# Kernel optimization log

Hardware: AMD Instinct MI355X
Metric: run time of the kernel (lower is better)

Reference implementation:

```python
import jax, jax.numpy as jnp
import numpy as np

N = 100000      # number of edge features (rows of feats)
M = 800000      # number of triplets
HID = 128
HEADS = 8
DH = HID // HEADS


def setup_inputs() -> dict:
    key = jax.random.key(0)
    ks = jax.random.split(key, 10)
    s = 1.0 / np.sqrt(HID)
    inp = {
        "feats": jax.random.normal(ks[0], (N, HID), dtype=jnp.float32),
        "idx_kj": jax.random.randint(ks[1], (M,), 0, N, dtype=jnp.int64),
        "idx_ji": jax.random.randint(ks[2], (M,), 0, N, dtype=jnp.int64),
        "Wv": jax.random.uniform(ks[3], (HID, HID), jnp.float32, -s, s),
        "Wq": jax.random.uniform(ks[4], (HID, HID), jnp.float32, -s, s),
        "Wk": jax.random.uniform(ks[5], (HID, HID), jnp.float32, -s, s),
        "W1": jax.random.uniform(ks[6], (HID, HID), jnp.float32, -s, s),
        "b1": jax.random.uniform(ks[7], (HID,), jnp.float32, -s, s),
        "W2": jax.random.uniform(ks[8], (HID, HID), jnp.float32, -s, s),
        "b2": jax.random.uniform(ks[9], (HID,), jnp.float32, -s, s),
    }
    return inp


def reference(feats, idx_kj, idx_ji, Wv, Wq, Wk, W1, b1, W2, b2):
    # Projections (no bias), reshape to [N, H, Dh]
    v = (feats @ Wv.T).reshape(N, HEADS, DH)
    k = (feats @ Wk.T).reshape(N, HEADS, DH)
    q = (feats @ Wq.T).reshape(N, HEADS, DH)

    # edge-indexed attention scores: [M, H, 1]
    att = jnp.sum(q[idx_kj] * k[idx_ji], axis=-1, keepdims=True)
    att = jnp.exp(jax.nn.leaky_relu(att, negative_slope=0.2))  # unsafe softmax, as in source

    # segment-sum normalizer over destination index idx_ji: [N, H, 1]
    denom = jax.ops.segment_sum(att, idx_ji, num_segments=N)
    att = att / denom[idx_ji]

    # weighted V gather-scatter: [M, HID] -> [N, HID]
    v_att = (v[idx_kj] * att).reshape(M, HID)
    agg = jax.ops.segment_sum(v_att, idx_ji, num_segments=N)  # v_clone after +scatter-v

    v_flat = v.reshape(N, HID)
    # ResidualLayer (dropout in eval mode -> identity): v + relu(lin2(relu(lin1(agg))))
    h = jax.nn.relu(agg @ W1.T + b1)
    h = jax.nn.relu(h @ W2.T + b2)
    return v_flat + h
```

## Files before the change

kernel.cpp:

```cpp
#include <hip/hip_runtime.h>
#include <hip/hip_bf16.h>
#include <math.h>

#define N_NODES 100000
#define M_EDGES 800000
#define HID 128
#define HEADS 8
#define DH 16
#define SCAN_NB ((N_NODES + 1023) / 1024)
#define DBINS 64

typedef __attribute__((ext_vector_type(8))) short short8;
typedef __attribute__((ext_vector_type(4))) float floatx4;

__device__ __forceinline__ ushort f32_to_bf16(float x) {
    __hip_bfloat16 h = __float2bfloat16(x);
    union { __hip_bfloat16 h; ushort u; } c; c.h = h;
    return c.u;
}
__device__ __forceinline__ float bf16_bits_to_f32(ushort u) {
    union { unsigned int i; float f; } c; c.i = ((unsigned int)u) << 16;
    return c.f;
}
__device__ __forceinline__ float bf16pair_lo(unsigned int p) {
    union { unsigned int i; float f; } c; c.i = p << 16; return c.f;
}
__device__ __forceinline__ float bf16pair_hi(unsigned int p) {
    union { unsigned int i; float f; } c; c.i = p & 0xffff0000u; return c.f;
}

__device__ __forceinline__ void stage_w_frag(const ushort* __restrict__ W,
                                             ushort* __restrict__ lds, int tid)
{
    #pragma unroll
    for (int i = 0; i < 8; ++i) {
        int idx  = i * 256 + tid;
        int f    = idx >> 6;
        int lane = idx & 63;
        int t    = f & 7, ks = f >> 3;
        int row  = t * 16 + (lane & 15);
        int col  = ks * 32 + (lane >> 4) * 8;
        uint4 d = *(const uint4*)(W + row * HID + col);
        *(uint4*)(lds + idx * 8) = d;
    }
}

__global__ __launch_bounds__(256) void cvt_w_kernel(
    const float* __restrict__ Wq, const float* __restrict__ Wk, const float* __restrict__ Wv,
    const float* __restrict__ W1, const float* __restrict__ W2,
    ushort* __restrict__ dq, ushort* __restrict__ dk, ushort* __restrict__ dv,
    ushort* __restrict__ d1, ushort* __restrict__ d2)
{
    int i = blockIdx.x * 256 + threadIdx.x;
    int w = i >> 14;
    int j = i & 16383;
    const float* s[5] = {Wq, Wk, Wv, W1, W2};
    ushort*      d[5] = {dq, dk, dv, d1, d2};
    d[w][j] = f32_to_bf16(s[w][j]);
}

__global__ __launch_bounds__(256) void qkv_mfma_kernel(
    const float* __restrict__ feats,
    const ushort* __restrict__ Wq16, const ushort* __restrict__ Wk16, const ushort* __restrict__ Wv16,
    ushort* __restrict__ qv16, ushort* __restrict__ k16)
{
    __shared__ ushort wlds[16384];
    const int tid  = threadIdx.x;
    const int wave = tid >> 6;
    const int lane = tid & 63;
    const int row0 = blockIdx.x * 128 + wave * 32;
    const int lrow = lane & 15;
    const int lk   = (lane >> 4) * 8;
    const int crow = (lane >> 4) * 4;

    short8 afrag[2][4];
    bool tvalid[2];
    #pragma unroll
    for (int r = 0; r < 2; ++r) {
        int rr = row0 + r * 16;
        tvalid[r] = (rr < N_NODES);
        const float* arow = feats + (size_t)((tvalid[r] ? rr : 0) + lrow) * HID + lk;
        #pragma unroll
        for (int ks = 0; ks < 4; ++ks) {
            float4 f0 = *(const float4*)(arow + ks * 32);
            float4 f1 = *(const float4*)(arow + ks * 32 + 4);
            short8 a;
            a[0] = (short)f32_to_bf16(f0.x); a[1] = (short)f32_to_bf16(f0.y);
            a[2] = (short)f32_to_bf16(f0.z); a[3] = (short)f32_to_bf16(f0.w);
            a[4] = (short)f32_to_bf16(f1.x); a[5] = (short)f32_to_bf16(f1.y);
            a[6] = (short)f32_to_bf16(f1.z); a[7] = (short)f32_to_bf16(f1.w);
            afrag[r][ks] = a;
        }
    }

    const ushort* Ws[3] = {Wq16, Wk16, Wv16};
    ushort* Ob[3]; int Ostride[3];
    Ob[0] = qv16;       Ostride[0] = 256;
    Ob[1] = k16;        Ostride[1] = 128;
    Ob[2] = qv16 + 128; Ostride[2] = 256;

    #pragma unroll
    for (int w = 0; w < 3; ++w) {
        __syncthreads();
        stage_w_frag(Ws[w], wlds, tid);
        __syncthreads();

        floatx4 acc[2][8];
        #pragma unroll
        for (int r = 0; r < 2; ++r)
            #pragma unroll
            for (int t = 0; t < 8; ++t) acc[r][t] = (floatx4)(0.f);

        #pragma unroll
        for (int ks = 0; ks < 4; ++ks) {
            short8 B[8];
            #pragma unroll
            for (int t = 0; t < 8; ++t)
                B[t] = *(const short8*)&wlds[(ks * 8 + t) * 512 + lane * 8];
            #pragma unroll
            for (int t = 0; t < 8; ++t) {
                acc[0][t] = __builtin_amdgcn_mfma_f32_16x16x32_bf16(B[t], afrag[0][ks], acc[0][t], 0, 0, 0);
                acc[1][t] = __builtin_amdgcn_mfma_f32_16x16x32_bf16(B[t], afrag[1][ks], acc[1][t], 0, 0, 0);
            }
        }

        #pragma unroll
        for (int r = 0; r < 2; ++r) {
            if (tvalid[r]) {
                ushort* O = Ob[w] + (size_t)(row0 + r * 16 + lrow) * Ostride[w];
                #pragma unroll
                for (int t = 0; t < 8; ++t) {
                    ushort4 o;
                    o.x = f32_to_bf16(acc[r][t][0]); o.y = f32_to_bf16(acc[r][t][1]);
                    o.z = f32_to_bf16(acc[r][t][2]); o.w = f32_to_bf16(acc[r][t][3]);
                    *(ushort4*)(O + t * 16 + crow) = o;
                }
            }
        }
    }
}

__global__ __launch_bounds__(256) void hist_kernel(
    const int* __restrict__ idx_ji, int* __restrict__ count)
{
    int m = blockIdx.x * 256 + threadIdx.x;
    if (m < M_EDGES) atomicAdd(&count[idx_ji[m]], 1);
}

__global__ __launch_bounds__(256) void scan_blocksum_kernel(
    const int* __restrict__ count, int* __restrict__ blocksum)
{
    __shared__ int s[256];
    const int tid = threadIdx.x;
    const int base = blockIdx.x * 1024 + tid * 4;
    int sum = 0;
    if (base + 3 < N_NODES) {
        int4 c = *(const int4*)(count + base);
        sum = c.x + c.y + c.z + c.w;
    } else {
        #pragma unroll
        for (int j = 0; j < 4; ++j) if (base + j < N_NODES) sum += count[base + j];
    }
    s[tid] = sum;
    __syncthreads();
    for (int off = 128; off > 0; off >>= 1) {
        if (tid < off) s[tid] += s[tid + off];
        __syncthreads();
    }
    if (tid == 0) blocksum[blockIdx.x] = s[0];
}

__global__ __launch_bounds__(128) void scan_top_kernel(int* __restrict__ blocksum)
{
    __shared__ int s[128];
    const int t = threadIdx.x;
    int v = (t < SCAN_NB) ? blocksum[t] : 0;
    s[t] = v;
    __syncthreads();
    for (int off = 1; off < 128; off <<= 1) {
        int x = (t >= off) ? s[t - off] : 0;
        __syncthreads();
        s[t] += x;
        __syncthreads();
    }
    if (t < SCAN_NB) blocksum[t] = s[t] - v;
}

__global__ __launch_bounds__(256) void scan_write_kernel(
    const int* __restrict__ count, const int* __restrict__ blocksum,
    int* __restrict__ offsets, int* __restrict__ cursor)
{
    __shared__ int s[256];
    const int tid = threadIdx.x;
    const int base = blockIdx.x * 1024 + tid * 4;
    int c0 = 0, c1 = 0, c2 = 0, c3 = 0;
    if (base + 3 < N_NODES) {
        int4 c = *(const int4*)(count + base);
        c0 = c.x; c1 = c.y; c2 = c.z; c3 = c.w;
    } else {
        if (base     < N_NODES) c0 = count[base];
        if (base + 1 < N_NODES) c1 = count[base + 1];
        if (base + 2 < N_NODES) c2 = count[base + 2];
        if (base + 3 < N_NODES) c3 = count[base + 3];
    }
    const int tsum = c0 + c1 + c2 + c3;
    s[tid] = tsum;
    __syncthreads();
    for (int off = 1; off < 256; off <<= 1) {
        int x = (tid >= off) ? s[tid - off] : 0;
        __syncthreads();
        s[tid] += x;
        __syncthreads();
    }
    int o0 = s[tid] - tsum + blocksum[blockIdx.x];
    int o1 = o0 + c0, o2 = o1 + c1, o3 = o2 + c2;
    if (base + 3 < N_NODES) {
        *(int4*)(offsets + base) = make_int4(o0, o1, o2, o3);
        *(int4*)(cursor  + base) = make_int4(o0, o1, o2, o3);
    } else {
        if (base     < N_NODES) { offsets[base]     = o0; cursor[base]     = o0; }
        if (base + 1 < N_NODES) { offsets[base + 1] = o1; cursor[base + 1] = o1; }
        if (base + 2 < N_NODES) { offsets[base + 2] = o2; cursor[base + 2] = o2; }
        if (base + 3 < N_NODES) { offsets[base + 3] = o3; cursor[base + 3] = o3; }
    }
}

__global__ __launch_bounds__(256) void fill_kernel(
    const int* __restrict__ idx_ji, const int* __restrict__ idx_kj,
    int* __restrict__ cursor, int* __restrict__ edge_kj)
{
    int m = blockIdx.x * 256 + threadIdx.x;
    if (m < M_EDGES) {
        int pos = atomicAdd(&cursor[idx_ji[m]], 1);
        edge_kj[pos] = idx_kj[m];
    }
}

__global__ __launch_bounds__(256) void deg_hist_kernel(
    const int* __restrict__ count, int* __restrict__ dhist)
{
    __shared__ int h[DBINS];
    const int tid = threadIdx.x;
    if (tid < DBINS) h[tid] = 0;
    __syncthreads();
    int n = blockIdx.x * 256 + tid;
    if (n < N_NODES) atomicAdd(&h[min(count[n], DBINS - 1)], 1);
    __syncthreads();
    if (tid < DBINS && h[tid]) atomicAdd(&dhist[tid], h[tid]);
}

__global__ __launch_bounds__(64) void deg_scan_kernel(
    const int* __restrict__ dhist, int* __restrict__ dcursor)
{
    __shared__ int s[DBINS];
    const int t = threadIdx.x;
    int v = dhist[t];
    s[t] = v;
    __syncthreads();
    for (int off = 1; off < DBINS; off <<= 1) {
        int x = (t >= off) ? s[t - off] : 0;
        __syncthreads();
        s[t] += x;
        __syncthreads();
    }
    dcursor[t] = s[t] - v;
}

__global__ __launch_bounds__(256) void deg_scatter_kernel(
    const int* __restrict__ count, int* __restrict__ dcursor,
    int* __restrict__ perm)
{
    __shared__ int h[DBINS];
    __shared__ int b[DBINS];
    const int tid = threadIdx.x;
    if (tid < DBINS) h[tid] = 0;
    __syncthreads();
    int n = blockIdx.x * 256 + tid;
    int d = -1, r = 0;
    if (n < N_NODES) {
        d = min(count[n], DBINS - 1);
        r = atomicAdd(&h[d], 1);
    }
    __syncthreads();
    if (tid < DBINS && h[tid]) b[tid] = atomicAdd(&dcursor[tid], h[tid]);
    __syncthreads();
    if (n < N_NODES) perm[b[d] + r] = n;
}

__device__ __forceinline__ float dot8(const uint4& qp, const float* kn) {
    const unsigned int* q = (const unsigned int*)&qp;
    float p = 0.f;
    #pragma unroll
    for (int j = 0; j < 4; ++j)
        p += bf16pair_lo(q[j]) * kn[2*j] + bf16pair_hi(q[j]) * kn[2*j+1];
    return p;
}
__device__ __forceinline__ void axpy8(float* acc, float s, const uint4& vp) {
    const unsigned int* v = (const unsigned int*)&vp;
    #pragma unroll
    for (int j = 0; j < 4; ++j) {
        acc[2*j]   += s * bf16pair_lo(v[j]);
        acc[2*j+1] += s * bf16pair_hi(v[j]);
    }
}

__global__ __launch_bounds__(256) void aggregate_kernel(
    const int* __restrict__ edge_kj, const int* __restrict__ offsets,
    const int* __restrict__ count, const int* __restrict__ perm,
    const ushort* __restrict__ qv16,
    const ushort* __restrict__ k16, ushort* __restrict__ agg16)
{
    const int gid  = blockIdx.x * 256 + threadIdx.x;
    const int slot = gid >> 4;
    const int l16  = threadIdx.x & 15;
    if (slot >= N_NODES) return;
    const int node = perm[slot];

    const int deg  = count[node];
    const int base = offsets[node];

    float kn[8];
    {
        uint4 kp = *(const uint4*)(k16 + (size_t)node * HID + l16 * 8);
        const unsigned int* kw = (const unsigned int*)&kp;
        #pragma unroll
        for (int j = 0; j < 4; ++j) {
            kn[2*j]   = bf16pair_lo(kw[j]);
            kn[2*j+1] = bf16pair_hi(kw[j]);
        }
    }

    float acc[8] = {0.f,0.f,0.f,0.f,0.f,0.f,0.f,0.f};
    float d = 0.f;

    const ushort* qvb = qv16 + l16 * 8;

    int e = 0;
    for (; e + 4 <= deg; e += 4) {
        const int kj0 = edge_kj[base + e + 0];
        const int kj1 = edge_kj[base + e + 1];
        const int kj2 = edge_kj[base + e + 2];
        const int kj3 = edge_kj[base + e + 3];
        const ushort* r0 = qvb + (size_t)kj0 * 256;
        const ushort* r1 = qvb + (size_t)kj1 * 256;
        const ushort* r2 = qvb + (size_t)kj2 * 256;
        const ushort* r3 = qvb + (size_t)kj3 * 256;
        uint4 qp0 = *(const uint4*)r0;  uint4 vp0 = *(const uint4*)(r0 + 128);
        uint4 qp1 = *(const uint4*)r1;  uint4 vp1 = *(const uint4*)(r1 + 128);
        uint4 qp2 = *(const uint4*)r2;  uint4 vp2 = *(const uint4*)(r2 + 128);
        uint4 qp3 = *(const uint4*)r3;  uint4 vp3 = *(const uint4*)(r3 + 128);

        float p0 = dot8(qp0, kn);
        float p1 = dot8(qp1, kn);
        float p2 = dot8(qp2, kn);
        float p3 = dot8(qp3, kn);
        p0 += __shfl_xor(p0, 1);
        p1 += __shfl_xor(p1, 1);
        p2 += __shfl_xor(p2, 1);
        p3 += __shfl_xor(p3, 1);
        float s0 = __expf(fmaxf(p0, 0.2f * p0));
        float s1 = __expf(fmaxf(p1, 0.2f * p1));
        float s2 = __expf(fmaxf(p2, 0.2f * p2));
        float s3 = __expf(fmaxf(p3, 0.2f * p3));
        d += (s0 + s1) + (s2 + s3);
        axpy8(acc, s0, vp0);
        axpy8(acc, s1, vp1);
        axpy8(acc, s2, vp2);
        axpy8(acc, s3, vp3);
    }
    if (e + 2 <= deg) {
        const int kj0 = edge_kj[base + e];
        const int kj1 = edge_kj[base + e + 1];
        const ushort* r0 = qvb + (size_t)kj0 * 256;
        const ushort* r1 = qvb + (size_t)kj1 * 256;
        uint4 qp0 = *(const uint4*)r0;  uint4 vp0 = *(const uint4*)(r0 + 128);
        uint4 qp1 = *(const uint4*)r1;  uint4 vp1 = *(const uint4*)(r1 + 128);
        float p0 = dot8(qp0, kn);
        float p1 = dot8(qp1, kn);
        p0 += __shfl_xor(p0, 1);
        p1 += __shfl_xor(p1, 1);
        float s0 = __expf(fmaxf(p0, 0.2f * p0));
        float s1 = __expf(fmaxf(p1, 0.2f * p1));
        d += s0 + s1;
        axpy8(acc, s0, vp0);
        axpy8(acc, s1, vp1);
        e += 2;
    }
    if (e < deg) {
        const int kj0 = edge_kj[base + e];
        const ushort* r0 = qvb + (size_t)kj0 * 256;
        uint4 qp0 = *(const uint4*)r0;  uint4 vp0 = *(const uint4*)(r0 + 128);
        float p0 = dot8(qp0, kn);
        p0 += __shfl_xor(p0, 1);
        float s0 = __expf(fmaxf(p0, 0.2f * p0));
        d += s0;
        axpy8(acc, s0, vp0);
    }

    const float inv = (deg > 0) ? 1.f / d : 0.f;
    uint4 o;
    unsigned int* ow = (unsigned int*)&o;
    #pragma unroll
    for (int j = 0; j < 4; ++j)
        ow[j] = (unsigned int)f32_to_bf16(acc[2*j] * inv)
              | ((unsigned int)f32_to_bf16(acc[2*j+1] * inv) << 16);
    *(uint4*)(agg16 + (size_t)node * HID + l16 * 8) = o;
}

__global__ __launch_bounds__(256) void mlp_mfma_kernel(
    const ushort* __restrict__ agg16, const ushort* __restrict__ qv16,
    const ushort* __restrict__ W1_16, const float* __restrict__ b1,
    const ushort* __restrict__ W2_16, const float* __restrict__ b2,
    float* __restrict__ out)
{
    __shared__ ushort wlds[16384];
    __shared__ ushort h1s[16384];
    const int tid  = threadIdx.x;
    const int wave = tid >> 6;
    const int lane = tid & 63;
    const int row0 = blockIdx.x * 128 + wave * 32;
    const int lrow = lane & 15;
    const int lk   = (lane >> 4) * 8;
    const int crow = (lane >> 4) * 4;

    short8 afrag[2][4];
    bool tvalid[2];
    #pragma unroll
    for (int r = 0; r < 2; ++r) {
        int rr = row0 + r * 16;
        tvalid[r] = (rr < N_NODES);
        const ushort* arow = agg16 + (size_t)((tvalid[r] ? rr : 0) + lrow) * HID + lk;
        #pragma unroll
        for (int ks = 0; ks < 4; ++ks)
            afrag[r][ks] = *(const short8*)(arow + ks * 32);
    }

    stage_w_frag(W1_16, wlds, tid);
    __syncthreads();

    {
        floatx4 acc[2][8];
        #pragma unroll
        for (int r = 0; r < 2; ++r)
            #pragma unroll
            for (int t = 0; t < 8; ++t) acc[r][t] = (floatx4)(0.f);
        #pragma unroll
        for (int ks = 0; ks < 4; ++ks) {
            short8 B[8];
            #pragma unroll
            for (int t = 0; t < 8; ++t)
                B[t] = *(const short8*)&wlds[(ks * 8 + t) * 512 + lane * 8];
            #pragma unroll
            for (int t = 0; t < 8; ++t) {
                acc[0][t] = __builtin_amdgcn_mfma_f32_16x16x32_bf16(B[t], afrag[0][ks], acc[0][t], 0, 0, 0);
                acc[1][t] = __builtin_amdgcn_mfma_f32_16x16x32_bf16(B[t], afrag[1][ks], acc[1][t], 0, 0, 0);
            }
        }
        #pragma unroll
        for (int r = 0; r < 2; ++r) {
            ushort* tile = &h1s[(wave * 2 + r) * 2048];
            #pragma unroll
            for (int t = 0; t < 8; ++t) {
                float4 bias = *(const float4*)(b1 + t * 16 + crow);
                ushort4 o;
                o.x = f32_to_bf16(fmaxf(acc[r][t][0] + bias.x, 0.f));
                o.y = f32_to_bf16(fmaxf(acc[r][t][1] + bias.y, 0.f));
                o.z = f32_to_bf16(fmaxf(acc[r][t][2] + bias.z, 0.f));
                o.w = f32_to_bf16(fmaxf(acc[r][t][3] + bias.w, 0.f));
                int ks   = t >> 1;
                int quad = (t & 1) * 2 + (crow >> 3);
                int j0   = crow & 4;
                *(ushort4*)(tile + (ks * 64 + quad * 16 + lrow) * 8 + j0) = o;
            }
        }
    }
    __syncthreads();
    stage_w_frag(W2_16, wlds, tid);
    __syncthreads();

    {
        short8 hfrag[2][4];
        #pragma unroll
        for (int r = 0; r < 2; ++r) {
            const ushort* tile = &h1s[(wave * 2 + r) * 2048];
            #pragma unroll
            for (int ks = 0; ks < 4; ++ks)
                hfrag[r][ks] = *(const short8*)(tile + (ks * 64 + lane) * 8);
        }
        floatx4 acc[2][8];
        #pragma unroll
        for (int r = 0; r < 2; ++r)
            #pragma unroll
            for (int t = 0; t < 8; ++t) acc[r][t] = (floatx4)(0.f);
        #pragma unroll
        for (int ks = 0; ks < 4; ++ks) {
            short8 B[8];
            #pragma unroll
            for (int t = 0; t < 8; ++t)
                B[t] = *(const short8*)&wlds[(ks * 8 + t) * 512 + lane * 8];
            #pragma unroll
            for (int t = 0; t < 8; ++t) {
                acc[0][t] = __builtin_amdgcn_mfma_f32_16x16x32_bf16(B[t], hfrag[0][ks], acc[0][t], 0, 0, 0);
                acc[1][t] = __builtin_amdgcn_mfma_f32_16x16x32_bf16(B[t], hfrag[1][ks], acc[1][t], 0, 0, 0);
            }
        }
        #pragma unroll
        for (int r = 0; r < 2; ++r) {
            if (tvalid[r]) {
                const size_t nrow = (size_t)(row0 + r * 16 + lrow);
                const ushort* vrow = qv16 + nrow * 256 + 128;
                float* orow = out + nrow * HID;
                #pragma unroll
                for (int t = 0; t < 8; ++t) {
                    float4 bias = *(const float4*)(b2 + t * 16 + crow);
                    ushort4 vv = *(const ushort4*)(vrow + t * 16 + crow);
                    float4 o;
                    o.x = bf16_bits_to_f32(vv.x) + fmaxf(acc[r][t][0] + bias.x, 0.f);
                    o.y = bf16_bits_to_f32(vv.y) + fmaxf(acc[r][t][1] + bias.y, 0.f);
                    o.z = bf16_bits_to_f32(vv.z) + fmaxf(acc[r][t][2] + bias.z, 0.f);
                    o.w = bf16_bits_to_f32(vv.w) + fmaxf(acc[r][t][3] + bias.w, 0.f);
                    *(float4*)(orow + t * 16 + crow) = o;
                }
            }
        }
    }
}

extern "C" void kernel_launch(void* const* d_in, const int* in_sizes, int n_in,
                              void* d_out, int out_size, void* d_ws, size_t ws_size,
                              hipStream_t stream) {
    const float* feats  = (const float*)d_in[0];
    const int*   idx_kj = (const int*)d_in[1];
    const int*   idx_ji = (const int*)d_in[2];
    const float* Wv     = (const float*)d_in[3];
    const float* Wq     = (const float*)d_in[4];
    const float* Wk     = (const float*)d_in[5];
    const float* W1     = (const float*)d_in[6];
    const float* b1     = (const float*)d_in[7];
    const float* W2     = (const float*)d_in[8];
    const float* b2     = (const float*)d_in[9];
    float* out = (float*)d_out;

    ushort* qv16    = (ushort*)d_ws;
    ushort* k16     = qv16    + (size_t)N_NODES * 256;
    ushort* agg16   = k16     + (size_t)N_NODES * HID;
    ushort* Wq16    = agg16   + (size_t)N_NODES * HID;
    ushort* Wk16    = Wq16 + HID * HID;
    ushort* Wv16    = Wk16 + HID * HID;
    ushort* W116    = Wv16 + HID * HID;
    ushort* W216    = W116 + HID * HID;
    int* count      = (int*)(W216 + HID * HID);
    int* offsets    = count + N_NODES;
    int* cursor     = offsets + N_NODES;
    int* blocksum   = cursor + N_NODES;
    int* edge_kj    = blocksum + ((SCAN_NB + 3) & ~3);
    int* dhist      = edge_kj + M_EDGES;
    int* dcursor    = dhist + DBINS;
    int* perm       = cursor;

    hipMemsetAsync(count, 0, N_NODES * sizeof(int), stream);
    hipMemsetAsync(dhist, 0, DBINS * sizeof(int), stream);

    cvt_w_kernel<<<(5 * HID * HID + 255) / 256, 256, 0, stream>>>(
        Wq, Wk, Wv, W1, W2, Wq16, Wk16, Wv16, W116, W216);

    qkv_mfma_kernel<<<(N_NODES + 127) / 128, 256, 0, stream>>>(
        feats, Wq16, Wk16, Wv16, qv16, k16);

    hist_kernel<<<(M_EDGES + 255) / 256, 256, 0, stream>>>(idx_ji, count);
    scan_blocksum_kernel<<<SCAN_NB, 256, 0, stream>>>(count, blocksum);
    scan_top_kernel<<<1, 128, 0, stream>>>(blocksum);
    scan_write_kernel<<<SCAN_NB, 256, 0, stream>>>(count, blocksum, offsets, cursor);
    fill_kernel<<<(M_EDGES + 255) / 256, 256, 0, stream>>>(idx_ji, idx_kj, cursor, edge_kj);

    deg_hist_kernel<<<(N_NODES + 255) / 256, 256, 0, stream>>>(count, dhist);
    deg_scan_kernel<<<1, DBINS, 0, stream>>>(dhist, dcursor);
    deg_scatter_kernel<<<(N_NODES + 255) / 256, 256, 0, stream>>>(count, dcursor, perm);

    aggregate_kernel<<<((size_t)N_NODES * 16 + 255) / 256, 256, 0, stream>>>(
        edge_kj, offsets, count, perm, qv16, k16, agg16);

    mlp_mfma_kernel<<<(N_NODES + 127) / 128, 256, 0, stream>>>(
        agg16, qv16, W116, b1, W216, b2, out);
}
```

Measured before the change: 349.8 us.

## Pre-swizzle weights into MFMA fragment layout and drop degree-sort permutation

The weight conversion kernel now writes bf16 weights directly in the per-lane MFMA fragment order, so the QKV and MLP kernels read B fragments straight from global memory (L2-resident) instead of staging them through LDS with barriers. This frees 32 KB of LDS per block in the QKV and MLP kernels and removes their sync points. Separately, the degree-bucketing pass (histogram, scan, scatter into a permutation) is removed and aggregate processes nodes in natural order, saving three launches and a memset at the cost of worse load balance across wavefronts.

After: 335.0 us. -4.2%, faster.

```diff
diff --git a/kernel.cpp b/kernel.cpp
--- a/kernel.cpp
+++ b/kernel.cpp
@@ -8,7 +8,6 @@
 #define HEADS 8
 #define DH 16
 #define SCAN_NB ((N_NODES + 1023) / 1024)
-#define DBINS 64
 
 typedef __attribute__((ext_vector_type(8))) short short8;
 typedef __attribute__((ext_vector_type(4))) float floatx4;
@@ -27,22 +26,6 @@
 }
 __device__ __forceinline__ float bf16pair_hi(unsigned int p) {
     union { unsigned int i; float f; } c; c.i = p & 0xffff0000u; return c.f;
-}
-
-__device__ __forceinline__ void stage_w_frag(const ushort* __restrict__ W,
-                                             ushort* __restrict__ lds, int tid)
-{
-    #pragma unroll
-    for (int i = 0; i < 8; ++i) {
-        int idx  = i * 256 + tid;
-        int f    = idx >> 6;
-        int lane = idx & 63;
-        int t    = f & 7, ks = f >> 3;
-        int row  = t * 16 + (lane & 15);
-        int col  = ks * 32 + (lane >> 4) * 8;
-        uint4 d = *(const uint4*)(W + row * HID + col);
-        *(uint4*)(lds + idx * 8) = d;
-    }
 }
 
 __global__ __launch_bounds__(256) void cvt_w_kernel(
@@ -53,10 +36,16 @@
 {
     int i = blockIdx.x * 256 + threadIdx.x;
     int w = i >> 14;
-    int j = i & 16383;
+    int o = i & 16383;
+    int j    = o & 7;
+    int lane = (o >> 3) & 63;
+    int f    = o >> 9;
+    int t    = f & 7, ks = f >> 3;
+    int row  = t * 16 + (lane & 15);
+    int col  = ks * 32 + (lane >> 4) * 8 + j;
     const float* s[5] = {Wq, Wk, Wv, W1, W2};
     ushort*      d[5] = {dq, dk, dv, d1, d2};
-    d[w][j] = f32_to_bf16(s[w][j]);
+    d[w][o] = f32_to_bf16(s[w][row * HID + col]);
 }
 
 __global__ __launch_bounds__(256) void qkv_mfma_kernel(
@@ -64,7 +53,6 @@
     const ushort* __restrict__ Wq16, const ushort* __restrict__ Wk16, const ushort* __restrict__ Wv16,
     ushort* __restrict__ qv16, ushort* __restrict__ k16)
 {
-    __shared__ ushort wlds[16384];
     const int tid  = threadIdx.x;
     const int wave = tid >> 6;
     const int lane = tid & 63;
@@ -101,9 +89,7 @@
 
     #pragma unroll
     for (int w = 0; w < 3; ++w) {
-        __syncthreads();
-        stage_w_frag(Ws[w], wlds, tid);
-        __syncthreads();
+        const ushort* Wf = Ws[w];
 
         floatx4 acc[2][8];
         #pragma unroll
@@ -116,7 +102,7 @@
             short8 B[8];
             #pragma unroll
             for (int t = 0; t < 8; ++t)
-                B[t] = *(const short8*)&wlds[(ks * 8 + t) * 512 + lane * 8];
+                B[t] = *(const short8*)&Wf[(ks * 8 + t) * 512 + lane * 8];
             #pragma unroll
             for (int t = 0; t < 8; ++t) {
                 acc[0][t] = __builtin_amdgcn_mfma_f32_16x16x32_bf16(B[t], afrag[0][ks], acc[0][t], 0, 0, 0);
@@ -236,57 +222,6 @@
     }
 }
 
-__global__ __launch_bounds__(256) void deg_hist_kernel(
-    const int* __restrict__ count, int* __restrict__ dhist)
-{
-    __shared__ int h[DBINS];
-    const int tid = threadIdx.x;
-    if (tid < DBINS) h[tid] = 0;
-    __syncthreads();
-    int n = blockIdx.x * 256 + tid;
-    if (n < N_NODES) atomicAdd(&h[min(count[n], DBINS - 1)], 1);
-    __syncthreads();
-    if (tid < DBINS && h[tid]) atomicAdd(&dhist[tid], h[tid]);
-}
-
-__global__ __launch_bounds__(64) void deg_scan_kernel(
-    const int* __restrict__ dhist, int* __restrict__ dcursor)
-{
-    __shared__ int s[DBINS];
-    const int t = threadIdx.x;
-    int v = dhist[t];
-    s[t] = v;
-    __syncthreads();
-    for (int off = 1; off < DBINS; off <<= 1) {
-        int x = (t >= off) ? s[t - off] : 0;
-        __syncthreads();
-        s[t] += x;
-        __syncthreads();
-    }
-    dcursor[t] = s[t] - v;
-}
-
-__global__ __launch_bounds__(256) void deg_scatter_kernel(
-    const int* __restrict__ count, int* __restrict__ dcursor,
-    int* __restrict__ perm)
-{
-    __shared__ int h[DBINS];
-    __shared__ int b[DBINS];
-    const int tid = threadIdx.x;
-    if (tid < DBINS) h[tid] = 0;
-    __syncthreads();
-    int n = blockIdx.x * 256 + tid;
-    int d = -1, r = 0;
-    if (n < N_NODES) {
-        d = min(count[n], DBINS - 1);
-        r = atomicAdd(&h[d], 1);
-    }
-    __syncthreads();
-    if (tid < DBINS && h[tid]) b[tid] = atomicAdd(&dcursor[tid], h[tid]);
-    __syncthreads();
-    if (n < N_NODES) perm[b[d] + r] = n;
-}
-
 __device__ __forceinline__ float dot8(const uint4& qp, const float* kn) {
     const unsigned int* q = (const unsigned int*)&qp;
     float p = 0.f;
@@ -306,15 +241,13 @@
 
 __global__ __launch_bounds__(256) void aggregate_kernel(
     const int* __restrict__ edge_kj, const int* __restrict__ offsets,
-    const int* __restrict__ count, const int* __restrict__ perm,
-    const ushort* __restrict__ qv16,
+    const int* __restrict__ count, const ushort* __restrict__ qv16,
     const ushort* __restrict__ k16, ushort* __restrict__ agg16)
 {
     const int gid  = blockIdx.x * 256 + threadIdx.x;
-    const int slot = gid >> 4;
+    const int node = gid >> 4;
     const int l16  = threadIdx.x & 15;
-    if (slot >= N_NODES) return;
-    const int node = perm[slot];
+    if (node >= N_NODES) return;
 
     const int deg  = count[node];
     const int base = offsets[node];
@@ -413,7 +346,6 @@
     const ushort* __restrict__ W2_16, const float* __restrict__ b2,
     float* __restrict__ out)
 {
-    __shared__ ushort wlds[16384];
     __shared__ ushort h1s[16384];
     const int tid  = threadIdx.x;
     const int wave = tid >> 6;
@@ -435,9 +367,6 @@
             afrag[r][ks] = *(const short8*)(arow + ks * 32);
     }
 
-    stage_w_frag(W1_16, wlds, tid);
-    __syncthreads();
-
     {
         floatx4 acc[2][8];
         #pragma unroll
@@ -449,7 +378,7 @@
             short8 B[8];
             #pragma unroll
             for (int t = 0; t < 8; ++t)
-                B[t] = *(const short8*)&wlds[(ks * 8 + t) * 512 + lane * 8];
+                B[t] = *(const short8*)&W1_16[(ks * 8 + t) * 512 + lane * 8];
             #pragma unroll
             for (int t = 0; t < 8; ++t) {
                 acc[0][t] = __builtin_amdgcn_mfma_f32_16x16x32_bf16(B[t], afrag[0][ks], acc[0][t], 0, 0, 0);
@@ -475,8 +404,6 @@
         }
     }
     __syncthreads();
-    stage_w_frag(W2_16, wlds, tid);
-    __syncthreads();
 
     {
         short8 hfrag[2][4];
@@ -497,7 +424,7 @@
             short8 B[8];
             #pragma unroll
             for (int t = 0; t < 8; ++t)
-                B[t] = *(const short8*)&wlds[(ks * 8 + t) * 512 + lane * 8];
+                B[t] = *(const short8*)&W2_16[(ks * 8 + t) * 512 + lane * 8];
             #pragma unroll
             for (int t = 0; t < 8; ++t) {
                 acc[0][t] = __builtin_amdgcn_mfma_f32_16x16x32_bf16(B[t], hfrag[0][ks], acc[0][t], 0, 0, 0);
@@ -554,12 +481,8 @@
     int* cursor     = offsets + N_NODES;
     int* blocksum   = cursor + N_NODES;
     int* edge_kj    = blocksum + ((SCAN_NB + 3) & ~3);
-    int* dhist      = edge_kj + M_EDGES;
-    int* dcursor    = dhist + DBINS;
-    int* perm       = cursor;
 
     hipMemsetAsync(count, 0, N_NODES * sizeof(int), stream);
-    hipMemsetAsync(dhist, 0, DBINS * sizeof(int), stream);
 
     cvt_w_kernel<<<(5 * HID * HID + 255) / 256, 256, 0, stream>>>(
         Wq, Wk, Wv, W1, W2, Wq16, Wk16, Wv16, W116, W216);
@@ -573,12 +496,8 @@
     scan_write_kernel<<<SCAN_NB, 256, 0, stream>>>(count, blocksum, offsets, cursor);
     fill_kernel<<<(M_EDGES + 255) / 256, 256, 0, stream>>>(idx_ji, idx_kj, cursor, edge_kj);
 
-    deg_hist_kernel<<<(N_NODES + 255) / 256, 256, 0, stream>>>(count, dhist);
-    deg_scan_kernel<<<1, DBINS, 0, stream>>>(dhist, dcursor);
-    deg_scatter_kernel<<<(N_NODES + 255) / 256, 256, 0, stream>>>(count, dcursor, perm);
-
     aggregate_kernel<<<((size_t)N_NODES * 16 + 255) / 256, 256, 0, stream>>>(
-        edge_kj, offsets, count, perm, qv16, k16, agg16);
+        edge_kj, offsets, count, qv16, k16, agg16);
 
     mlp_mfma_kernel<<<(N_NODES + 127) / 128, 256, 0, stream>>>(
         agg16, qv16, W116, b1, W216, b2, out);
```
